# Kernel optimization log

Hardware: AMD Instinct MI355X
Metric: run time of the kernel (lower is better)

## Reference

```python
import jax, jax.numpy as jnp
import numpy as np

B, T, D, H, K = 2, 384, 512, 8, 48
HD = D // H  # head_dim = 64
LN_EPS = 1e-5


def setup_inputs() -> dict:
    key = jax.random.key(0)
    ks = jax.random.split(key, 6)
    def lin_w(k, out_d, in_d):
        return jax.random.normal(k, (out_d, in_d), jnp.float32) / np.sqrt(in_d).astype(np.float32)
    return {
        "x": jax.random.normal(ks[0], (B, T, D), jnp.float32),
        "g_w": lin_w(ks[1], H, D), "g_b": jnp.zeros((H,), jnp.float32),
        "sp_w": lin_w(ks[2], D, HD), "sp_b": jnp.zeros((D,), jnp.float32),
        "gate_w": lin_w(ks[3], D, D), "gate_b": jnp.zeros((D,), jnp.float32),
        "U_w": lin_w(ks[4], D, D), "U_b": jnp.zeros((D,), jnp.float32),
        "ln_g": jnp.ones((D,), jnp.float32), "ln_b": jnp.zeros((D,), jnp.float32),
    }


def reference(x, g_w, g_b, sp_w, sp_b, gate_w, gate_b, U_w, U_b, ln_g, ln_b):
    b, t, d = x.shape
    # head-split superposition
    phi = x.reshape(b, t, H, HD)                               # (B,T,H,hd)
    alpha = jax.nn.softmax(x @ g_w.T + g_b, axis=-1)           # (B,T,H)
    x_super = jnp.einsum('bth,bthd->btd', alpha, phi)          # (B,T,hd)
    x_super = x_super @ sp_w.T + sp_b                          # (B,T,D)
    # gated pairwise entanglement: interaction[b,i,j,:] = gate[b,i]*gate[b,j]
    gate = jax.nn.sigmoid(x_super @ gate_w.T + gate_b)         # (B,T,D)
    interaction = gate[:, :, None, :] * gate[:, None, :, :]    # (B,T,T,D)
    # top-k by L2 norm over feature dim, gather along j axis
    scores = jnp.sqrt(jnp.sum(interaction * interaction, axis=-1))  # (B,T,T)
    _, idx = jax.lax.top_k(scores, K)                          # (B,T,K)
    gathered = jnp.take_along_axis(interaction, idx[..., None], axis=2)  # (B,T,K,D)
    entangled = gathered.sum(axis=2)                           # (B,T,D)
    x_out = x_super + entangled
    y = x_out @ U_w.T + U_b
    mu = jnp.mean(y, axis=-1, keepdims=True)
    var = jnp.mean((y - mu) ** 2, axis=-1, keepdims=True)
    return ln_g * (y - mu) * jax.lax.rsqrt(var + LN_EPS) + ln_b
```

## Files before the change

### kernel.cpp

```cpp
#include <hip/hip_runtime.h>
#include <math.h>
#include <float.h>

#define B_ 2
#define T_ 384
#define D_ 512
#define H_ 8
#define HD_ 64
#define K_ 48
#define LN_EPS 1e-5f
#define NTOK (B_ * T_)
#define PART_STRIDE (NTOK * D_)
#define T2 (T_ * T_)

__global__ __launch_bounds__(256) void k_super(const float* __restrict__ x,
                                               const float* __restrict__ g_w,
                                               const float* __restrict__ g_b,
                                               const float* __restrict__ sp_w,
                                               const float* __restrict__ sp_b,
                                               float* __restrict__ xs) {
    int token = blockIdx.x;
    int tid = threadIdx.x;
    __shared__ float xsh[D_];
    __shared__ float logits[H_];
    __shared__ float hd[HD_];
    const float* xt = x + (size_t)token * D_;
    ((float2*)xsh)[tid] = ((const float2*)xt)[tid];
    __syncthreads();
    int h = tid >> 5, l = tid & 31;
    float p = 0.f;
#pragma unroll
    for (int i = 0; i < 16; ++i) {
        int k = l + 32 * i;
        p += xsh[k] * g_w[h * D_ + k];
    }
#pragma unroll
    for (int off = 16; off > 0; off >>= 1) p += __shfl_xor(p, off);
    if (l == 0) logits[h] = p + g_b[h];
    __syncthreads();
    if (tid < HD_) {
        float m = logits[0];
#pragma unroll
        for (int hh = 1; hh < H_; ++hh) m = fmaxf(m, logits[hh]);
        float e[H_];
        float sum = 0.f;
#pragma unroll
        for (int hh = 0; hh < H_; ++hh) { e[hh] = expf(logits[hh] - m); sum += e[hh]; }
        float inv = 1.f / sum;
        float v = 0.f;
#pragma unroll
        for (int hh = 0; hh < H_; ++hh) v += e[hh] * inv * xsh[hh * HD_ + tid];
        hd[tid] = v;
    }
    __syncthreads();
    float a0 = sp_b[tid], a1 = sp_b[tid + 256];
    const float* w0 = sp_w + (size_t)tid * HD_;
    const float* w1 = sp_w + (size_t)(tid + 256) * HD_;
#pragma unroll
    for (int k = 0; k < HD_; k += 4) {
        float4 h4 = *(const float4*)&hd[k];
        float4 u0 = *(const float4*)&w0[k];
        float4 u1 = *(const float4*)&w1[k];
        a0 += h4.x * u0.x + h4.y * u0.y + h4.z * u0.z + h4.w * u0.w;
        a1 += h4.x * u1.x + h4.y * u1.y + h4.z * u1.z + h4.w * u1.w;
    }
    xs[(size_t)token * D_ + tid] = a0;
    xs[(size_t)token * D_ + 256 + tid] = a1;
}

__global__ __launch_bounds__(256) void k_wgemm_part(const float* __restrict__ in,
                                                    const float* __restrict__ W,
                                                    float* __restrict__ part) {
    int c0 = blockIdx.x * 64, r0 = blockIdx.y * 32;
    int kbase = blockIdx.z * 64;
    float* pout = part + (size_t)blockIdx.z * PART_STRIDE;
    int tid = threadIdx.x;
    int ry = tid >> 4, cx = tid & 15;
    __shared__ float A_shT[32][33];
    __shared__ float B_sh[32][65];
    float acc[2][4];
#pragma unroll
    for (int r = 0; r < 2; ++r)
#pragma unroll
        for (int c = 0; c < 4; ++c) acc[r][c] = 0.f;
    int asr = tid >> 3, asc = (tid & 7) * 4;
    int bsr = tid >> 2, bsk = (tid & 3) * 8;
    for (int k0 = kbase; k0 < kbase + 64; k0 += 32) {
        float4 a4 = *(const float4*)&in[(size_t)(r0 + asr) * D_ + k0 + asc];
        A_shT[asc + 0][asr] = a4.x;
        A_shT[asc + 1][asr] = a4.y;
        A_shT[asc + 2][asr] = a4.z;
        A_shT[asc + 3][asr] = a4.w;
        float4 b4a = *(const float4*)&W[(size_t)(c0 + bsr) * D_ + k0 + bsk];
        float4 b4b = *(const float4*)&W[(size_t)(c0 + bsr) * D_ + k0 + bsk + 4];
        B_sh[bsk + 0][bsr] = b4a.x;
        B_sh[bsk + 1][bsr] = b4a.y;
        B_sh[bsk + 2][bsr] = b4a.z;
        B_sh[bsk + 3][bsr] = b4a.w;
        B_sh[bsk + 4][bsr] = b4b.x;
        B_sh[bsk + 5][bsr] = b4b.y;
        B_sh[bsk + 6][bsr] = b4b.z;
        B_sh[bsk + 7][bsr] = b4b.w;
        __syncthreads();
#pragma unroll
        for (int kk = 0; kk < 32; ++kk) {
            float2 a2 = *(const float2*)&A_shT[kk][ry * 2];
            float4 b4 = *(const float4*)&B_sh[kk][cx * 4];
            acc[0][0] += a2.x * b4.x; acc[0][1] += a2.x * b4.y;
            acc[0][2] += a2.x * b4.z; acc[0][3] += a2.x * b4.w;
            acc[1][0] += a2.y * b4.x; acc[1][1] += a2.y * b4.y;
            acc[1][2] += a2.y * b4.z; acc[1][3] += a2.y * b4.w;
        }
        __syncthreads();
    }
#pragma unroll
    for (int r = 0; r < 2; ++r) {
        float4 o;
        o.x = acc[r][0];
        o.y = acc[r][1];
        o.z = acc[r][2];
        o.w = acc[r][3];
        *(float4*)&pout[(size_t)(r0 + ry * 2 + r) * D_ + c0 + cx * 4] = o;
    }
}

__global__ __launch_bounds__(256) void k_wred_sig(const float* __restrict__ part,
                                                  const float* __restrict__ bias,
                                                  float* __restrict__ out) {
    int idx = blockIdx.x * 256 + threadIdx.x;
    const float4* p = (const float4*)part;
    float4 s = {0.f, 0.f, 0.f, 0.f};
#pragma unroll
    for (int q = 0; q < 8; ++q) {
        float4 a = p[idx + q * (PART_STRIDE / 4)];
        s.x += a.x; s.y += a.y; s.z += a.z; s.w += a.w;
    }
    float4 bb = ((const float4*)bias)[idx & 127];
    s.x = 1.f / (1.f + expf(-(s.x + bb.x)));
    s.y = 1.f / (1.f + expf(-(s.y + bb.y)));
    s.z = 1.f / (1.f + expf(-(s.z + bb.z)));
    s.w = 1.f / (1.f + expf(-(s.w + bb.w)));
    ((float4*)out)[idx] = s;
}

__global__ __launch_bounds__(256) void k_scores_part(const float* __restrict__ gate,
                                                     float* __restrict__ spart) {
    int z = blockIdx.z;
    int b = z >> 3, ks = z & 7;
    int kbase = ks * 64;
    int i0 = blockIdx.y * 64, j0 = blockIdx.x * 64;
    int tid = threadIdx.x;
    int tx = tid & 15, ty = tid >> 4;
    __shared__ float Ash[16][68];
    __shared__ float Bsh[16][68];
    float acc[4][4];
#pragma unroll
    for (int r = 0; r < 4; ++r)
#pragma unroll
        for (int c = 0; c < 4; ++c) acc[r][c] = 0.f;
    const float* gb = gate + (size_t)b * T_ * D_;
    int sr = tid >> 2, sc4 = (tid & 3) * 4;
    for (int k0 = kbase; k0 < kbase + 64; k0 += 16) {
        float4 av = *(const float4*)&gb[(size_t)(i0 + sr) * D_ + k0 + sc4];
        float4 bvv = *(const float4*)&gb[(size_t)(j0 + sr) * D_ + k0 + sc4];
        Ash[sc4 + 0][sr] = av.x * av.x;
        Ash[sc4 + 1][sr] = av.y * av.y;
        Ash[sc4 + 2][sr] = av.z * av.z;
        Ash[sc4 + 3][sr] = av.w * av.w;
        Bsh[sc4 + 0][sr] = bvv.x * bvv.x;
        Bsh[sc4 + 1][sr] = bvv.y * bvv.y;
        Bsh[sc4 + 2][sr] = bvv.z * bvv.z;
        Bsh[sc4 + 3][sr] = bvv.w * bvv.w;
        __syncthreads();
#pragma unroll
        for (int kk = 0; kk < 16; ++kk) {
            float4 a4 = *(const float4*)&Ash[kk][4 * ty];
            float4 b4 = *(const float4*)&Bsh[kk][4 * tx];
            float ar[4] = {a4.x, a4.y, a4.z, a4.w};
            float bc[4] = {b4.x, b4.y, b4.z, b4.w};
#pragma unroll
            for (int r = 0; r < 4; ++r)
#pragma unroll
                for (int c = 0; c < 4; ++c) acc[r][c] += ar[r] * bc[c];
        }
        __syncthreads();
    }
    float* sp = spart + (size_t)z * T2;
#pragma unroll
    for (int r = 0; r < 4; ++r) {
        float4 o;
        o.x = acc[r][0];
        o.y = acc[r][1];
        o.z = acc[r][2];
        o.w = acc[r][3];
        *(float4*)&sp[(size_t)(i0 + 4 * ty + r) * T_ + j0 + 4 * tx] = o;
    }
}

__global__ __launch_bounds__(64) void k_topk_ent(const float* __restrict__ spart,
                                                 const float* __restrict__ gate,
                                                 const float* __restrict__ xs,
                                                 float* __restrict__ xo) {
    int row = blockIdx.x;
    int b = row / T_;
    int i = row - b * T_;
    int lane = threadIdx.x;
    float v[6];
#pragma unroll
    for (int q = 0; q < 6; ++q) {
        float s = 0.f;
#pragma unroll
        for (int ks = 0; ks < 8; ++ks)
            s += spart[(size_t)(b * 8 + ks) * T2 + (size_t)i * T_ + q * 64 + lane];
        v[q] = sqrtf(s);
    }
    int keep = 0;
    for (int it = 0; it < K_; ++it) {
        float bv = v[0];
        int bq = 0;
#pragma unroll
        for (int q = 1; q < 6; ++q)
            if (v[q] > bv) { bv = v[q]; bq = q; }
        int bidx = bq * 64 + lane;
#pragma unroll
        for (int off = 1; off < 64; off <<= 1) {
            float ov = __shfl_xor(bv, off);
            int oi = __shfl_xor(bidx, off);
            if (ov > bv || (ov == bv && oi < bidx)) { bv = ov; bidx = oi; }
        }
        if (lane == (bidx & 63)) v[bidx >> 6] = -FLT_MAX;
        if (lane == it) keep = bidx;
    }
    float4 s0 = {0.f, 0.f, 0.f, 0.f}, s1 = {0.f, 0.f, 0.f, 0.f};
    const float* gb = gate + (size_t)b * T_ * D_;
    for (int n = 0; n < K_; ++n) {
        int j = __shfl(keep, n);
        const float4* gj = (const float4*)(gb + (size_t)j * D_ + lane * 8);
        float4 g0 = gj[0], g1 = gj[1];
        s0.x += g0.x; s0.y += g0.y; s0.z += g0.z; s0.w += g0.w;
        s1.x += g1.x; s1.y += g1.y; s1.z += g1.z; s1.w += g1.w;
    }
    size_t base = (size_t)row * D_ + lane * 8;
    const float4* gi = (const float4*)(gate + base);
    const float4* xi = (const float4*)(xs + base);
    float4 gi0 = gi[0], gi1 = gi[1];
    float4 x0 = xi[0], x1 = xi[1];
    x0.x += gi0.x * s0.x; x0.y += gi0.y * s0.y; x0.z += gi0.z * s0.z; x0.w += gi0.w * s0.w;
    x1.x += gi1.x * s1.x; x1.y += gi1.y * s1.y; x1.z += gi1.z * s1.z; x1.w += gi1.w * s1.w;
    float4* xov = (float4*)(xo + base);
    xov[0] = x0;
    xov[1] = x1;
}

__global__ __launch_bounds__(256) void k_wred_ln(const float* __restrict__ part,
                                                 const float* __restrict__ U_b,
                                                 const float* __restrict__ ln_g,
                                                 const float* __restrict__ ln_b,
                                                 float* __restrict__ out) {
    int tid = threadIdx.x;
    int idx = blockIdx.x * 256 + tid;
    const float4* p = (const float4*)part;
    float4 s = {0.f, 0.f, 0.f, 0.f};
#pragma unroll
    for (int q = 0; q < 8; ++q) {
        float4 a = p[idx + q * (PART_STRIDE / 4)];
        s.x += a.x; s.y += a.y; s.z += a.z; s.w += a.w;
    }
    float4 ub = ((const float4*)U_b)[tid & 127];
    s.x += ub.x; s.y += ub.y; s.z += ub.z; s.w += ub.w;
    float sum = s.x + s.y + s.z + s.w;
    float sq = s.x * s.x + s.y * s.y + s.z * s.z + s.w * s.w;
#pragma unroll
    for (int off = 32; off > 0; off >>= 1) {
        sum += __shfl_xor(sum, off);
        sq += __shfl_xor(sq, off);
    }
    __shared__ float red[4][2];
    int wave = tid >> 6;
    if ((tid & 63) == 0) { red[wave][0] = sum; red[wave][1] = sq; }
    __syncthreads();
    int rw = (tid >> 7) * 2;
    float m1 = red[rw][0] + red[rw + 1][0];
    float m2 = red[rw][1] + red[rw + 1][1];
    float mu = m1 * (1.f / D_);
    float var = fmaxf(m2 * (1.f / D_) - mu * mu, 0.f);
    float inv = rsqrtf(var + LN_EPS);
    float4 lg = ((const float4*)ln_g)[tid & 127];
    float4 lb = ((const float4*)ln_b)[tid & 127];
    float4 o;
    o.x = lg.x * (s.x - mu) * inv + lb.x;
    o.y = lg.y * (s.y - mu) * inv + lb.y;
    o.z = lg.z * (s.z - mu) * inv + lb.z;
    o.w = lg.w * (s.w - mu) * inv + lb.w;
    ((float4*)out)[idx] = o;
}

extern "C" void kernel_launch(void* const* d_in, const int* in_sizes, int n_in,
                              void* d_out, int out_size, void* d_ws, size_t ws_size,
                              hipStream_t stream) {
    const float* x      = (const float*)d_in[0];
    const float* g_w    = (const float*)d_in[1];
    const float* g_b    = (const float*)d_in[2];
    const float* sp_w   = (const float*)d_in[3];
    const float* sp_b   = (const float*)d_in[4];
    const float* gate_w = (const float*)d_in[5];
    const float* gate_b = (const float*)d_in[6];
    const float* U_w    = (const float*)d_in[7];
    const float* U_b    = (const float*)d_in[8];
    const float* ln_g   = (const float*)d_in[9];
    const float* ln_b   = (const float*)d_in[10];

    float* ws    = (float*)d_ws;
    float* xs    = ws;
    float* gate  = xs + 393216;
    float* xo    = gate + 393216;
    float* part  = xo + 393216;
    float* spart = part + 8 * 393216;

    k_super<<<NTOK, 256, 0, stream>>>(x, g_w, g_b, sp_w, sp_b, xs);
    k_wgemm_part<<<dim3(D_ / 64, NTOK / 32, 8), 256, 0, stream>>>(xs, gate_w, part);
    k_wred_sig<<<NTOK * D_ / 1024, 256, 0, stream>>>(part, gate_b, gate);
    k_scores_part<<<dim3(T_ / 64, T_ / 64, 16), 256, 0, stream>>>(gate, spart);
    k_topk_ent<<<NTOK, 64, 0, stream>>>(spart, gate, xs, xo);
    k_wgemm_part<<<dim3(D_ / 64, NTOK / 32, 8), 256, 0, stream>>>(xo, U_w, part);
    k_wred_ln<<<NTOK * D_ / 1024, 256, 0, stream>>>(part, U_b, ln_g, ln_b, (float*)d_out);
}
```

Baseline: 181.0 us.

## Fold sp_w into gate_w, rank-based topk, fewer split-K partials

Precomputes the combined matrix gate_w·sp_w (512x64) and its bias inside the superposition kernel, so the gate GEMM becomes a rank-64 product over the head-dim vector instead of a full 512x512 GEMM with split-K partials and a reduction pass. Top-k is replaced by a rank-counting selection over squared scores in a 256-thread block, dropping the sqrt and the iterative wave argmax. The U GEMM split-K factor drops from 8 to 4. Together these remove one kernel and shrink partial-sum traffic. The cost is a different floating-point summation order, and the O(T^2) counting loop per row does more comparisons than the old selection.

```diff
diff --git a/kernel.cpp b/kernel.cpp
--- a/kernel.cpp
+++ b/kernel.cpp
@@ -2,78 +2,221 @@
 #include <math.h>
 #include <float.h>
 
-#define B_ 2
 #define T_ 384
 #define D_ 512
 #define H_ 8
 #define HD_ 64
 #define K_ 48
 #define LN_EPS 1e-5f
-#define NTOK (B_ * T_)
-#define PART_STRIDE (NTOK * D_)
+#define NTOK 768
+#define PSTRIDE (NTOK * D_)
 #define T2 (T_ * T_)
 
-__global__ __launch_bounds__(256) void k_super(const float* __restrict__ x,
-                                               const float* __restrict__ g_w,
-                                               const float* __restrict__ g_b,
-                                               const float* __restrict__ sp_w,
-                                               const float* __restrict__ sp_b,
-                                               float* __restrict__ xs) {
-    int token = blockIdx.x;
-    int tid = threadIdx.x;
+__global__ __launch_bounds__(256) void k_super_m(
+    const float* __restrict__ x, const float* __restrict__ g_w,
+    const float* __restrict__ g_b, const float* __restrict__ sp_w,
+    const float* __restrict__ sp_b, const float* __restrict__ gate_w,
+    const float* __restrict__ gate_b, float* __restrict__ xs,
+    float* __restrict__ hd_g, float* __restrict__ MT, float* __restrict__ Mb) {
     __shared__ float xsh[D_];
     __shared__ float logits[H_];
-    __shared__ float hd[HD_];
-    const float* xt = x + (size_t)token * D_;
-    ((float2*)xsh)[tid] = ((const float2*)xt)[tid];
+    __shared__ float hdv[HD_];
+    int bid = blockIdx.x, tid = threadIdx.x;
+    if (bid < NTOK) {
+        const float* xt = x + (size_t)bid * D_;
+        ((float2*)xsh)[tid] = ((const float2*)xt)[tid];
+        __syncthreads();
+        int h = tid >> 5, l = tid & 31;
+        float p = 0.f;
+#pragma unroll
+        for (int i = 0; i < 16; ++i) {
+            int k = l + 32 * i;
+            p += xsh[k] * g_w[h * D_ + k];
+        }
+#pragma unroll
+        for (int off = 16; off > 0; off >>= 1) p += __shfl_xor(p, off);
+        if (l == 0) logits[h] = p + g_b[h];
+        __syncthreads();
+        if (tid < HD_) {
+            float m = logits[0];
+#pragma unroll
+            for (int hh = 1; hh < H_; ++hh) m = fmaxf(m, logits[hh]);
+            float e[H_];
+            float sum = 0.f;
+#pragma unroll
+            for (int hh = 0; hh < H_; ++hh) { e[hh] = expf(logits[hh] - m); sum += e[hh]; }
+            float inv = 1.f / sum;
+            float v = 0.f;
+#pragma unroll
+            for (int hh = 0; hh < H_; ++hh) v += e[hh] * inv * xsh[hh * HD_ + tid];
+            hdv[tid] = v;
+            hd_g[(size_t)bid * HD_ + tid] = v;
+        }
+        __syncthreads();
+        float a0 = sp_b[tid], a1 = sp_b[tid + 256];
+        const float* w0 = sp_w + (size_t)tid * HD_;
+        const float* w1 = sp_w + (size_t)(tid + 256) * HD_;
+#pragma unroll
+        for (int k = 0; k < HD_; k += 4) {
+            float4 h4 = *(const float4*)&hdv[k];
+            float4 u0 = *(const float4*)&w0[k];
+            float4 u1 = *(const float4*)&w1[k];
+            a0 += h4.x * u0.x + h4.y * u0.y + h4.z * u0.z + h4.w * u0.w;
+            a1 += h4.x * u1.x + h4.y * u1.y + h4.z * u1.z + h4.w * u1.w;
+        }
+        xs[(size_t)bid * D_ + tid] = a0;
+        xs[(size_t)bid * D_ + 256 + tid] = a1;
+    } else {
+        int d = (bid - NTOK) * 4 + (tid >> 6);
+        int l = tid & 63;
+        const float* gw = gate_w + (size_t)d * D_;
+        float p = 0.f;
+#pragma unroll
+        for (int i = 0; i < 8; ++i) p += gw[l + 64 * i] * sp_b[l + 64 * i];
+#pragma unroll
+        for (int off = 32; off > 0; off >>= 1) p += __shfl_xor(p, off);
+        if (l == 0) Mb[d] = p + gate_b[d];
+        float acc = 0.f;
+        for (int k = 0; k < D_; k += 4) {
+            float4 a4 = *(const float4*)&gw[k];
+            acc += a4.x * sp_w[(k + 0) * HD_ + l] + a4.y * sp_w[(k + 1) * HD_ + l] +
+                   a4.z * sp_w[(k + 2) * HD_ + l] + a4.w * sp_w[(k + 3) * HD_ + l];
+        }
+        MT[(size_t)l * D_ + d] = acc;
+    }
+}
+
+__global__ __launch_bounds__(256) void k_gate(const float* __restrict__ hd_g,
+                                              const float* __restrict__ MT,
+                                              const float* __restrict__ Mb,
+                                              float* __restrict__ gate) {
+    int bid = blockIdx.x, tid = threadIdx.x;
+    int t0 = (bid >> 3) * 8, c0 = (bid & 7) * 64;
+    int rr = tid >> 6, c = tid & 63;
+    int ta = t0 + rr, tb = t0 + rr + 4;
+    const float4* hd4 = (const float4*)hd_g;
+    float acc0 = 0.f, acc1 = 0.f;
+#pragma unroll
+    for (int j4 = 0; j4 < 16; ++j4) {
+        float4 h0 = hd4[ta * 16 + j4];
+        float4 h1 = hd4[tb * 16 + j4];
+        int j = j4 * 4;
+        float m0 = MT[(size_t)(j + 0) * D_ + c0 + c];
+        float m1 = MT[(size_t)(j + 1) * D_ + c0 + c];
+        float m2 = MT[(size_t)(j + 2) * D_ + c0 + c];
+        float m3 = MT[(size_t)(j + 3) * D_ + c0 + c];
+        acc0 += h0.x * m0 + h0.y * m1 + h0.z * m2 + h0.w * m3;
+        acc1 += h1.x * m0 + h1.y * m1 + h1.z * m2 + h1.w * m3;
+    }
+    float mb = Mb[c0 + c];
+    gate[(size_t)ta * D_ + c0 + c] = 1.f / (1.f + expf(-(acc0 + mb)));
+    gate[(size_t)tb * D_ + c0 + c] = 1.f / (1.f + expf(-(acc1 + mb)));
+}
+
+__global__ __launch_bounds__(256) void k_scores_part(const float* __restrict__ gate,
+                                                     float* __restrict__ spart) {
+    int z = blockIdx.z;
+    int b = z >> 3, ks = z & 7;
+    int kbase = ks * 64;
+    int i0 = blockIdx.y * 64, j0 = blockIdx.x * 64;
+    int tid = threadIdx.x;
+    int tx = tid & 15, ty = tid >> 4;
+    __shared__ float Ash[16][68];
+    __shared__ float Bsh[16][68];
+    float acc[4][4];
+#pragma unroll
+    for (int r = 0; r < 4; ++r)
+#pragma unroll
+        for (int c = 0; c < 4; ++c) acc[r][c] = 0.f;
+    const float* gb = gate + (size_t)b * T_ * D_;
+    int sr = tid >> 2, sc4 = (tid & 3) * 4;
+    for (int k0 = kbase; k0 < kbase + 64; k0 += 16) {
+        float4 av = *(const float4*)&gb[(size_t)(i0 + sr) * D_ + k0 + sc4];
+        float4 bvv = *(const float4*)&gb[(size_t)(j0 + sr) * D_ + k0 + sc4];
+        Ash[sc4 + 0][sr] = av.x * av.x;
+        Ash[sc4 + 1][sr] = av.y * av.y;
+        Ash[sc4 + 2][sr] = av.z * av.z;
+        Ash[sc4 + 3][sr] = av.w * av.w;
+        Bsh[sc4 + 0][sr] = bvv.x * bvv.x;
+        Bsh[sc4 + 1][sr] = bvv.y * bvv.y;
+        Bsh[sc4 + 2][sr] = bvv.z * bvv.z;
+        Bsh[sc4 + 3][sr] = bvv.w * bvv.w;
+        __syncthreads();
+#pragma unroll
+        for (int kk = 0; kk < 16; ++kk) {
+            float4 a4 = *(const float4*)&Ash[kk][4 * ty];
+            float4 b4 = *(const float4*)&Bsh[kk][4 * tx];
+            float ar[4] = {a4.x, a4.y, a4.z, a4.w};
+            float bc[4] = {b4.x, b4.y, b4.z, b4.w};
+#pragma unroll
+            for (int r = 0; r < 4; ++r)
+#pragma unroll
+                for (int c = 0; c < 4; ++c) acc[r][c] += ar[r] * bc[c];
+        }
+        __syncthreads();
+    }
+    float* sp = spart + (size_t)z * T2;
+#pragma unroll
+    for (int r = 0; r < 4; ++r) {
+        float4 o;
+        o.x = acc[r][0];
+        o.y = acc[r][1];
+        o.z = acc[r][2];
+        o.w = acc[r][3];
+        *(float4*)&sp[(size_t)(i0 + 4 * ty + r) * T_ + j0 + 4 * tx] = o;
+    }
+}
+
+__global__ __launch_bounds__(256) void k_topk_ent(const float* __restrict__ spart,
+                                                  const float* __restrict__ gate,
+                                                  const float* __restrict__ xs,
+                                                  float* __restrict__ xo) {
+    __shared__ float s[T_];
+    __shared__ int sel[K_];
+    int row = blockIdx.x, tid = threadIdx.x;
+    int b = row / T_;
+    int i = row - b * T_;
+    for (int j = tid; j < T_; j += 256) {
+        float acc = 0.f;
+#pragma unroll
+        for (int ks = 0; ks < 8; ++ks)
+            acc += spart[(size_t)(b * 8 + ks) * T2 + (size_t)i * T_ + j];
+        s[j] = acc;
+    }
     __syncthreads();
-    int h = tid >> 5, l = tid & 31;
-    float p = 0.f;
-#pragma unroll
-    for (int i = 0; i < 16; ++i) {
-        int k = l + 32 * i;
-        p += xsh[k] * g_w[h * D_ + k];
-    }
-#pragma unroll
-    for (int off = 16; off > 0; off >>= 1) p += __shfl_xor(p, off);
-    if (l == 0) logits[h] = p + g_b[h];
+    for (int j = tid; j < T_; j += 256) {
+        float v = s[j];
+        int cnt = 0;
+        for (int j2 = 0; j2 < T_; ++j2) {
+            float u = s[j2];
+            cnt += (u > v) || (u == v && j2 < j);
+        }
+        if (cnt < K_) sel[cnt] = j;
+    }
     __syncthreads();
-    if (tid < HD_) {
-        float m = logits[0];
-#pragma unroll
-        for (int hh = 1; hh < H_; ++hh) m = fmaxf(m, logits[hh]);
-        float e[H_];
-        float sum = 0.f;
-#pragma unroll
-        for (int hh = 0; hh < H_; ++hh) { e[hh] = expf(logits[hh] - m); sum += e[hh]; }
-        float inv = 1.f / sum;
-        float v = 0.f;
-#pragma unroll
-        for (int hh = 0; hh < H_; ++hh) v += e[hh] * inv * xsh[hh * HD_ + tid];
-        hd[tid] = v;
-    }
-    __syncthreads();
-    float a0 = sp_b[tid], a1 = sp_b[tid + 256];
-    const float* w0 = sp_w + (size_t)tid * HD_;
-    const float* w1 = sp_w + (size_t)(tid + 256) * HD_;
-#pragma unroll
-    for (int k = 0; k < HD_; k += 4) {
-        float4 h4 = *(const float4*)&hd[k];
-        float4 u0 = *(const float4*)&w0[k];
-        float4 u1 = *(const float4*)&w1[k];
-        a0 += h4.x * u0.x + h4.y * u0.y + h4.z * u0.z + h4.w * u0.w;
-        a1 += h4.x * u1.x + h4.y * u1.y + h4.z * u1.z + h4.w * u1.w;
-    }
-    xs[(size_t)token * D_ + tid] = a0;
-    xs[(size_t)token * D_ + 256 + tid] = a1;
+    const float2* g2 = (const float2*)gate;
+    float2 sum = {0.f, 0.f};
+    int rb = b * T_;
+    for (int n = 0; n < K_; ++n) {
+        int j = sel[n];
+        float2 g = g2[(size_t)(rb + j) * 256 + tid];
+        sum.x += g.x;
+        sum.y += g.y;
+    }
+    float2 gi = g2[(size_t)row * 256 + tid];
+    float2 xv = ((const float2*)xs)[(size_t)row * 256 + tid];
+    float2 o;
+    o.x = xv.x + gi.x * sum.x;
+    o.y = xv.y + gi.y * sum.y;
+    ((float2*)xo)[(size_t)row * 256 + tid] = o;
 }
 
 __global__ __launch_bounds__(256) void k_wgemm_part(const float* __restrict__ in,
                                                     const float* __restrict__ W,
                                                     float* __restrict__ part) {
     int c0 = blockIdx.x * 64, r0 = blockIdx.y * 32;
-    int kbase = blockIdx.z * 64;
-    float* pout = part + (size_t)blockIdx.z * PART_STRIDE;
+    int kbase = blockIdx.z * 128;
+    float* pout = part + (size_t)blockIdx.z * PSTRIDE;
     int tid = threadIdx.x;
     int ry = tid >> 4, cx = tid & 15;
     __shared__ float A_shT[32][33];
@@ -85,7 +228,7 @@
         for (int c = 0; c < 4; ++c) acc[r][c] = 0.f;
     int asr = tid >> 3, asc = (tid & 7) * 4;
     int bsr = tid >> 2, bsk = (tid & 3) * 8;
-    for (int k0 = kbase; k0 < kbase + 64; k0 += 32) {
+    for (int k0 = kbase; k0 < kbase + 128; k0 += 32) {
         float4 a4 = *(const float4*)&in[(size_t)(r0 + asr) * D_ + k0 + asc];
         A_shT[asc + 0][asr] = a4.x;
         A_shT[asc + 1][asr] = a4.y;
@@ -124,134 +267,6 @@
     }
 }
 
-__global__ __launch_bounds__(256) void k_wred_sig(const float* __restrict__ part,
-                                                  const float* __restrict__ bias,
-                                                  float* __restrict__ out) {
-    int idx = blockIdx.x * 256 + threadIdx.x;
-    const float4* p = (const float4*)part;
-    float4 s = {0.f, 0.f, 0.f, 0.f};
-#pragma unroll
-    for (int q = 0; q < 8; ++q) {
-        float4 a = p[idx + q * (PART_STRIDE / 4)];
-        s.x += a.x; s.y += a.y; s.z += a.z; s.w += a.w;
-    }
-    float4 bb = ((const float4*)bias)[idx & 127];
-    s.x = 1.f / (1.f + expf(-(s.x + bb.x)));
-    s.y = 1.f / (1.f + expf(-(s.y + bb.y)));
-    s.z = 1.f / (1.f + expf(-(s.z + bb.z)));
-    s.w = 1.f / (1.f + expf(-(s.w + bb.w)));
-    ((float4*)out)[idx] = s;
-}
-
-__global__ __launch_bounds__(256) void k_scores_part(const float* __restrict__ gate,
-                                                     float* __restrict__ spart) {
-    int z = blockIdx.z;
-    int b = z >> 3, ks = z & 7;
-    int kbase = ks * 64;
-    int i0 = blockIdx.y * 64, j0 = blockIdx.x * 64;
-    int tid = threadIdx.x;
-    int tx = tid & 15, ty = tid >> 4;
-    __shared__ float Ash[16][68];
-    __shared__ float Bsh[16][68];
-    float acc[4][4];
-#pragma unroll
-    for (int r = 0; r < 4; ++r)
-#pragma unroll
-        for (int c = 0; c < 4; ++c) acc[r][c] = 0.f;
-    const float* gb = gate + (size_t)b * T_ * D_;
-    int sr = tid >> 2, sc4 = (tid & 3) * 4;
-    for (int k0 = kbase; k0 < kbase + 64; k0 += 16) {
-        float4 av = *(const float4*)&gb[(size_t)(i0 + sr) * D_ + k0 + sc4];
-        float4 bvv = *(const float4*)&gb[(size_t)(j0 + sr) * D_ + k0 + sc4];
-        Ash[sc4 + 0][sr] = av.x * av.x;
-        Ash[sc4 + 1][sr] = av.y * av.y;
-        Ash[sc4 + 2][sr] = av.z * av.z;
-        Ash[sc4 + 3][sr] = av.w * av.w;
-        Bsh[sc4 + 0][sr] = bvv.x * bvv.x;
-        Bsh[sc4 + 1][sr] = bvv.y * bvv.y;
-        Bsh[sc4 + 2][sr] = bvv.z * bvv.z;
-        Bsh[sc4 + 3][sr] = bvv.w * bvv.w;
-        __syncthreads();
-#pragma unroll
-        for (int kk = 0; kk < 16; ++kk) {
-            float4 a4 = *(const float4*)&Ash[kk][4 * ty];
-            float4 b4 = *(const float4*)&Bsh[kk][4 * tx];
-            float ar[4] = {a4.x, a4.y, a4.z, a4.w};
-            float bc[4] = {b4.x, b4.y, b4.z, b4.w};
-#pragma unroll
-            for (int r = 0; r < 4; ++r)
-#pragma unroll
-                for (int c = 0; c < 4; ++c) acc[r][c] += ar[r] * bc[c];
-        }
-        __syncthreads();
-    }
-    float* sp = spart + (size_t)z * T2;
-#pragma unroll
-    for (int r = 0; r < 4; ++r) {
-        float4 o;
-        o.x = acc[r][0];
-        o.y = acc[r][1];
-        o.z = acc[r][2];
-        o.w = acc[r][3];
-        *(float4*)&sp[(size_t)(i0 + 4 * ty + r) * T_ + j0 + 4 * tx] = o;
-    }
-}
-
-__global__ __launch_bounds__(64) void k_topk_ent(const float* __restrict__ spart,
-                                                 const float* __restrict__ gate,
-                                                 const float* __restrict__ xs,
-                                                 float* __restrict__ xo) {
-    int row = blockIdx.x;
-    int b = row / T_;
-    int i = row - b * T_;
-    int lane = threadIdx.x;
-    float v[6];
-#pragma unroll
-    for (int q = 0; q < 6; ++q) {
-        float s = 0.f;
-#pragma unroll
-        for (int ks = 0; ks < 8; ++ks)
-            s += spart[(size_t)(b * 8 + ks) * T2 + (size_t)i * T_ + q * 64 + lane];
-        v[q] = sqrtf(s);
-    }
-    int keep = 0;
-    for (int it = 0; it < K_; ++it) {
-        float bv = v[0];
-        int bq = 0;
-#pragma unroll
-        for (int q = 1; q < 6; ++q)
-            if (v[q] > bv) { bv = v[q]; bq = q; }
-        int bidx = bq * 64 + lane;
-#pragma unroll
-        for (int off = 1; off < 64; off <<= 1) {
-            float ov = __shfl_xor(bv, off);
-            int oi = __shfl_xor(bidx, off);
-            if (ov > bv || (ov == bv && oi < bidx)) { bv = ov; bidx = oi; }
-        }
-        if (lane == (bidx & 63)) v[bidx >> 6] = -FLT_MAX;
-        if (lane == it) keep = bidx;
-    }
-    float4 s0 = {0.f, 0.f, 0.f, 0.f}, s1 = {0.f, 0.f, 0.f, 0.f};
-    const float* gb = gate + (size_t)b * T_ * D_;
-    for (int n = 0; n < K_; ++n) {
-        int j = __shfl(keep, n);
-        const float4* gj = (const float4*)(gb + (size_t)j * D_ + lane * 8);
-        float4 g0 = gj[0], g1 = gj[1];
-        s0.x += g0.x; s0.y += g0.y; s0.z += g0.z; s0.w += g0.w;
-        s1.x += g1.x; s1.y += g1.y; s1.z += g1.z; s1.w += g1.w;
-    }
-    size_t base = (size_t)row * D_ + lane * 8;
-    const float4* gi = (const float4*)(gate + base);
-    const float4* xi = (const float4*)(xs + base);
-    float4 gi0 = gi[0], gi1 = gi[1];
-    float4 x0 = xi[0], x1 = xi[1];
-    x0.x += gi0.x * s0.x; x0.y += gi0.y * s0.y; x0.z += gi0.z * s0.z; x0.w += gi0.w * s0.w;
-    x1.x += gi1.x * s1.x; x1.y += gi1.y * s1.y; x1.z += gi1.z * s1.z; x1.w += gi1.w * s1.w;
-    float4* xov = (float4*)(xo + base);
-    xov[0] = x0;
-    xov[1] = x1;
-}
-
 __global__ __launch_bounds__(256) void k_wred_ln(const float* __restrict__ part,
                                                  const float* __restrict__ U_b,
                                                  const float* __restrict__ ln_g,
@@ -262,8 +277,8 @@
     const float4* p = (const float4*)part;
     float4 s = {0.f, 0.f, 0.f, 0.f};
 #pragma unroll
-    for (int q = 0; q < 8; ++q) {
-        float4 a = p[idx + q * (PART_STRIDE / 4)];
+    for (int q = 0; q < 4; ++q) {
+        float4 a = p[idx + q * (PSTRIDE / 4)];
         s.x += a.x; s.y += a.y; s.z += a.z; s.w += a.w;
     }
     float4 ub = ((const float4*)U_b)[tid & 127];
@@ -312,16 +327,19 @@
 
     float* ws    = (float*)d_ws;
     float* xs    = ws;
-    float* gate  = xs + 393216;
-    float* xo    = gate + 393216;
-    float* part  = xo + 393216;
-    float* spart = part + 8 * 393216;
-
-    k_super<<<NTOK, 256, 0, stream>>>(x, g_w, g_b, sp_w, sp_b, xs);
-    k_wgemm_part<<<dim3(D_ / 64, NTOK / 32, 8), 256, 0, stream>>>(xs, gate_w, part);
-    k_wred_sig<<<NTOK * D_ / 1024, 256, 0, stream>>>(part, gate_b, gate);
+    float* gate  = xs + PSTRIDE;
+    float* xo    = gate + PSTRIDE;
+    float* hd_g  = xo + PSTRIDE;
+    float* MT    = hd_g + 49152;
+    float* Mb    = MT + 32768;
+    float* part  = Mb + 512;
+    float* spart = part + 4 * PSTRIDE;
+
+    k_super_m<<<NTOK + 128, 256, 0, stream>>>(x, g_w, g_b, sp_w, sp_b, gate_w,
+                                              gate_b, xs, hd_g, MT, Mb);
+    k_gate<<<NTOK, 256, 0, stream>>>(hd_g, MT, Mb, gate);
     k_scores_part<<<dim3(T_ / 64, T_ / 64, 16), 256, 0, stream>>>(gate, spart);
-    k_topk_ent<<<NTOK, 64, 0, stream>>>(spart, gate, xs, xo);
-    k_wgemm_part<<<dim3(D_ / 64, NTOK / 32, 8), 256, 0, stream>>>(xo, U_w, part);
+    k_topk_ent<<<NTOK, 256, 0, stream>>>(spart, gate, xs, xo);
+    k_wgemm_part<<<dim3(D_ / 64, NTOK / 32, 4), 256, 0, stream>>>(xo, U_w, part);
     k_wred_ln<<<NTOK * D_ / 1024, 256, 0, stream>>>(part, U_b, ln_g, ln_b, (float*)d_out);
 }
```

Measured after the change: 166.6 us. 8.0% less time.
